# Kernel optimization log

Measured on AMD Instinct MI355X. Metric: run time of the kernel, lower is better.

The kernel has to match this reference:

```python
import jax, jax.numpy as jnp
from jax import lax
import numpy as np

B, C, H, W = 8, 256, 192, 192
ATT_K = 11
BN_EPS = 1e-5


def _dwconv(x, w, pad, stride=1):
    # x: NCHW, w: (C,1,kh,kw) depthwise
    return lax.conv_general_dilated(
        x, w, window_strides=(stride, stride), padding=pad,
        feature_group_count=x.shape[1],
        dimension_numbers=('NCHW', 'OIHW', 'NCHW'))


def _max_pool_3x3(x):
    return lax.reduce_window(x, -jnp.inf, lax.max,
                             (1, 1, 3, 3), (1, 1, 1, 1), 'SAME')


def _blur_pool(x, stride=3):
    # antialiased_cnns.BlurPool, filt_size=4: reflect pad [1,2,1,2], binomial 4x4, depthwise, stride 3
    c = x.shape[1]
    a = jnp.array([1., 3., 3., 1.], dtype=x.dtype)
    filt = (a[:, None] * a[None, :])
    filt = filt / jnp.sum(filt)
    w = jnp.tile(filt[None, None], (c, 1, 1, 1))  # (C,1,4,4)
    xp = jnp.pad(x, ((0, 0), (0, 0), (1, 2), (1, 2)), mode='reflect')
    return _dwconv(xp, w, 'VALID', stride=stride)


def _h_transform(x):
    b, c, h, w = x.shape
    x = jnp.pad(x, ((0, 0), (0, 0), (0, 0), (0, w)))
    x = x.reshape(b, c, -1)[..., :-w]
    return x.reshape(b, c, h, 2 * w - 1)


def _inv_h_transform(x):
    b, c, h, _ = x.shape  # last dim = 2h-1 (requires square)
    x = x.reshape(b, c, -1)
    x = jnp.pad(x, ((0, 0), (0, 0), (0, h)))
    x = x.reshape(b, c, h, 2 * h)
    return x[..., :h]


def _v_transform(x):
    return jnp.transpose(_h_transform(jnp.transpose(x, (0, 1, 3, 2))), (0, 1, 3, 2))


def _inv_v_transform(x):
    return jnp.transpose(_inv_h_transform(jnp.transpose(x, (0, 1, 3, 2))), (0, 1, 3, 2))


def setup_inputs() -> dict:
    key = jax.random.key(0)
    ks = jax.random.split(key, 5)
    pad = ATT_K // 2
    return {
        'x': jax.random.normal(ks[0], (B, C, H, W), dtype=jnp.float32),
        'w_h1': jax.random.normal(ks[1], (C, 1, ATT_K, 3), dtype=jnp.float32) * 0.1,
        'w_v1': jax.random.normal(ks[2], (C, 1, 3, ATT_K), dtype=jnp.float32) * 0.1,
        'w_h2': jax.random.normal(ks[3], (C, 1, ATT_K, 3), dtype=jnp.float32) * 0.1,
        'w_v2': jax.random.normal(ks[4], (C, 1, 3, ATT_K), dtype=jnp.float32) * 0.1,
        'bn_gamma': jnp.ones((C,), dtype=jnp.float32),
        'bn_beta': jnp.zeros((C,), dtype=jnp.float32),
        'bn_mean': jnp.zeros((C,), dtype=jnp.float32),
        'bn_var': jnp.ones((C,), dtype=jnp.float32),
    }


def reference(x, w_h1, w_v1, w_h2, w_v2, bn_gamma, bn_beta, bn_mean, bn_var):
    pad = ATT_K // 2
    b, c, h, w = x.shape

    x_tem = _max_pool_3x3(x)
    x_tem = _blur_pool(x_tem, stride=3)  # (B,C,64,64)

    x_h1 = _dwconv(x_tem, w_h1, ((pad, pad), (1, 1)))
    x_w1 = _dwconv(x_tem, w_v1, ((1, 1), (pad, pad)))

    # h == w (192 == 192): diagonal branch active
    x_h2 = _inv_h_transform(_dwconv(_h_transform(x_tem), w_h2, ((pad, pad), (1, 1))))
    x_w2 = _inv_v_transform(_dwconv(_v_transform(x_tem), w_v2, ((1, 1), (pad, pad))))

    s = x_h1 + x_w1 + x_h2 + x_w2
    # inference BatchNorm2d
    inv = bn_gamma / jnp.sqrt(bn_var + BN_EPS)
    att = (s - bn_mean[None, :, None, None]) * inv[None, :, None, None] + bn_beta[None, :, None, None]

    gate = jax.nn.sigmoid(att)
    # nearest interpolate to (h, w): idx = floor(i * in/out)
    ah, aw = gate.shape[2], gate.shape[3]
    idx_h = (jnp.arange(h) * ah) // h
    idx_w = (jnp.arange(w) * aw) // w
    gate_up = gate[:, :, idx_h][:, :, :, idx_w]

    return x[:, :c] * gate_up
```

## Files before the change

### kernel.cpp

```cpp
#include <hip/hip_runtime.h>
#include <hip/hip_fp16.h>
#include <math.h>

#define BN_EPS 1e-5f

__device__ __forceinline__ float max3f(float a, float b, float c) {
    return fmaxf(fmaxf(a, b), c);
}

__global__ __launch_bounds__(256, 8)
void mra_fused(const float* __restrict__ x,
               const float* __restrict__ wh1,
               const float* __restrict__ wv1,
               const float* __restrict__ wh2,
               const float* __restrict__ wv2,
               const float* __restrict__ bng,
               const float* __restrict__ bnb,
               const float* __restrict__ bnm,
               const float* __restrict__ bnv,
               float* __restrict__ out)
{
    __shared__ __align__(16) __half sxp_h[76][84];
    __shared__ __align__(16) float  rowbuf[4][2][192];

    const int plane = blockIdx.x;
    const int c     = plane & 255;
    const int tid   = threadIdx.x;
    const int lane  = tid & 63;
    const int wv    = tid >> 6;
    const float* __restrict__ xp = x   + (size_t)plane * 36864;
    float* __restrict__       op = out + (size_t)plane * 36864;

    {
        int* z = (int*)&sxp_h[0][0];
        #pragma unroll
        for (int i = 0; i < 13; ++i) {
            const int idx = tid + (i << 8);
            if (idx < (76 * 84 * 2) / 4) z[idx] = 0;
        }
    }
    __syncthreads();

    {
        const int P0 = wv << 4;
        float* rb0 = rowbuf[wv][0];
        float* rb1 = rowbuf[wv][1];
        const int i0 = (lane == 0) ? 1 : 3 * lane - 1;
        const int i1 = 3 * lane, i2 = 3 * lane + 1, i3 = 3 * lane + 2;
        const int r0 = 3 * P0 - 2;

        float4 ring[4];
        auto issue = [&](int k, float4* slot) {
            int r = r0 + k;
            r = r < 0 ? 0 : (r > 191 ? 191 : r);
            float4 v = make_float4(0.f, 0.f, 0.f, 0.f);
            if (lane < 48) v = *(const float4*)(xp + r * 192 + 4 * lane);
            *slot = v;
        };
        issue(0, &ring[0]); issue(1, &ring[1]);
        issue(2, &ring[2]); issue(3, &ring[3]);

        float h[3][4];
        float hb[3];
        float hbp = 0.f;

        #pragma unroll
        for (int k = 0; k < 51; ++k) {
            float4 v4 = ring[k & 3];
            if (k + 4 < 51) issue(k + 4, &ring[k & 3]);

            float nl = __shfl_up(v4.w, 1);
            float nr = __shfl_down(v4.x, 1);
            if (lane == 0)  nl = v4.x;
            if (lane == 47) nr = v4.w;
            float* rb = (k & 1) ? rb1 : rb0;
            if (lane < 48) {
                float4 hm;
                hm.x = max3f(nl,   v4.x, v4.y);
                hm.y = max3f(v4.x, v4.y, v4.z);
                hm.z = max3f(v4.y, v4.z, v4.w);
                hm.w = max3f(v4.z, v4.w, nr);
                *(float4*)(rb + 4 * lane) = hm;
            }
            __builtin_amdgcn_wave_barrier();
            float* hk = h[k % 3];
            hk[0] = rb[i0]; hk[1] = rb[i1]; hk[2] = rb[i2]; hk[3] = rb[i3];
            __builtin_amdgcn_wave_barrier();

            if (k >= 2) {
                const float* a = h[(k - 2) % 3];
                const float* b = h[(k - 1) % 3];
                const float* d = h[k % 3];
                const float e4 =
                      0.125f * max3f(a[0], b[0], d[0])
                    + 0.375f * max3f(a[1], b[1], d[1])
                    + 0.375f * max3f(a[2], b[2], d[2])
                    + 0.125f * max3f(a[3], b[3], d[3]);
                if (k == 2) {
                    hbp = e4;
                } else {
                    hb[k % 3] = e4;
                    if (k % 3 == 2) {
                        const int i = (k - 5) / 3;
                        float a_out;
                        if (i == 0 && wv == 0)
                            a_out = 0.375f * hb[0] + 0.5f * hb[1] + 0.125f * hb[2];
                        else
                            a_out = 0.125f * hbp + 0.375f * hb[0]
                                  + 0.375f * hb[1] + 0.125f * hb[2];
                        hbp = hb[2];
                        sxp_h[P0 + i + 6][lane + 8] = __float2half(a_out);
                    }
                }
            }
        }
    }
    __syncthreads();

    const int p  = tid >> 2;
    const int q0 = (tid & 3) << 4;
    float acc[16];
    #pragma unroll
    for (int i = 0; i < 16; ++i) acc[i] = 0.0f;

    const float* __restrict__ wh1p = wh1 + c * 33;
    const float* __restrict__ wv1p = wv1 + c * 33;
    const float* __restrict__ wh2p = wh2 + c * 33;
    const float* __restrict__ wv2p = wv2 + c * 33;

    #pragma unroll
    for (int e = -6; e <= 6; ++e) {
        float rbx[32];
        const __half* rowl = &sxp_h[p + e + 6][q0];
        #pragma unroll
        for (int u = 0; u < 8; ++u) {
            const __half2* h2p = (const __half2*)(rowl + 4 * u);
            const float2 f0 = __half22float2(h2p[0]);
            const float2 f1 = __half22float2(h2p[1]);
            rbx[4 * u + 0] = f0.x; rbx[4 * u + 1] = f0.y;
            rbx[4 * u + 2] = f1.x; rbx[4 * u + 3] = f1.y;
        }
        if (e >= -5 && e <= 5) {
            #pragma unroll
            for (int dw = -1; dw <= 1; ++dw) {
                const float wt = wh1p[(e + 5) * 3 + dw + 1];
                #pragma unroll
                for (int i = 0; i < 16; ++i) acc[i] += wt * rbx[i + dw + 8];
            }
            #pragma unroll
            for (int dw = -1; dw <= 1; ++dw) {
                const float wt = wh2p[(e + 5) * 3 + dw + 1];
                #pragma unroll
                for (int i = 0; i < 16; ++i) acc[i] += wt * rbx[i + dw - e + 8];
            }
        }
        if (e >= -1 && e <= 1) {
            #pragma unroll
            for (int dw = -5; dw <= 5; ++dw) {
                const float wt = wv1p[(e + 1) * 11 + dw + 5];
                #pragma unroll
                for (int i = 0; i < 16; ++i) acc[i] += wt * rbx[i + dw + 8];
            }
        }
        #pragma unroll
        for (int dh = -1; dh <= 1; ++dh) {
            const int dw = dh - e;
            if (dw >= -5 && dw <= 5) {
                const float wt = wv2p[(dh + 1) * 11 + dw + 5];
                #pragma unroll
                for (int i = 0; i < 16; ++i) acc[i] += wt * rbx[i + dh - e + 8];
            }
        }
    }

    const float inv = bng[c] * rsqrtf(bnv[c] + BN_EPS);
    const float mu  = bnm[c];
    const float bt  = bnb[c];
    __syncthreads();
    #pragma unroll
    for (int i = 0; i < 8; ++i) {
        const float a0 = (acc[2 * i]     - mu) * inv + bt;
        const float a1 = (acc[2 * i + 1] - mu) * inv + bt;
        const float g0 = 1.0f / (1.0f + __expf(-a0));
        const float g1 = 1.0f / (1.0f + __expf(-a1));
        *(__half2*)(&sxp_h[p + 6][q0 + 2 * i + 8]) = __floats2half2_rn(g0, g1);
    }
    __syncthreads();

    const float4* __restrict__ x4 = (const float4*)xp;
    float4* __restrict__       o4 = (float4*)op;
    int rowj[3], gcj[3], rrj[3];
    #pragma unroll
    for (int j = 0; j < 3; ++j) {
        const int idx0 = tid + (j << 8);
        const int rw   = idx0 / 48;
        const int c4   = idx0 - rw * 48;
        rowj[j] = rw;
        const int jb = c4 << 2;
        gcj[j] = jb / 3;
        rrj[j] = jb - 3 * gcj[j];
    }
    #pragma unroll
    for (int m = 0; m < 12; ++m) {
        #pragma unroll
        for (int j = 0; j < 3; ++j) {
            const int row = rowj[j] + (m << 4);
            const int idx = tid + ((m * 3 + j) << 8);
            const int gr  = row / 3 + 6;
            const float g0 = __half2float(sxp_h[gr][gcj[j] + 8]);
            const float g1 = __half2float(sxp_h[gr][gcj[j] + 9]);
            const float4 xv = x4[idx];
            float4 ov;
            const float s1 = (rrj[j] == 2) ? g1 : g0;
            const float s2 = (rrj[j] >= 1) ? g1 : g0;
            ov.x = xv.x * g0;
            ov.y = xv.y * s1;
            ov.z = xv.z * s2;
            ov.w = xv.w * g1;
            o4[idx] = ov;
        }
    }
}

extern "C" void kernel_launch(void* const* d_in, const int* in_sizes, int n_in,
                              void* d_out, int out_size, void* d_ws, size_t ws_size,
                              hipStream_t stream) {
    const float* x   = (const float*)d_in[0];
    const float* wh1 = (const float*)d_in[1];
    const float* wv1 = (const float*)d_in[2];
    const float* wh2 = (const float*)d_in[3];
    const float* wv2 = (const float*)d_in[4];
    const float* g   = (const float*)d_in[5];
    const float* b   = (const float*)d_in[6];
    const float* m   = (const float*)d_in[7];
    const float* v   = (const float*)d_in[8];

    mra_fused<<<dim3(8 * 256), dim3(256), 0, stream>>>(
        x, wh1, wv1, wh2, wv2, g, b, m, v, (float*)d_out);
}
```

Before: 175.1 us.

## Split each plane across two 128-thread blocks with recomputed halo rows

Each channel plane is now handled by two blocks of 128 threads, each covering half of the 64 pooled rows plus a 6-row halo. Each block recomputes the pooled halo rows itself. The goal is twice as many smaller blocks, for better occupancy and load balance with less shared memory per block. The cost is redundant max/blur pooling of the halo rows and extra global reads of x for the overlapping rows.

```diff
diff --git a/kernel.cpp b/kernel.cpp
--- a/kernel.cpp
+++ b/kernel.cpp
@@ -8,7 +8,7 @@
     return fmaxf(fmaxf(a, b), c);
 }
 
-__global__ __launch_bounds__(256, 8)
+__global__ __launch_bounds__(128, 8)
 void mra_fused(const float* __restrict__ x,
                const float* __restrict__ wh1,
                const float* __restrict__ wv1,
@@ -20,11 +20,14 @@
                const float* __restrict__ bnv,
                float* __restrict__ out)
 {
-    __shared__ __align__(16) __half sxp_h[76][84];
-    __shared__ __align__(16) float  rowbuf[4][2][192];
-
-    const int plane = blockIdx.x;
+    __shared__ __align__(16) __half sxp_h[44][84];
+    __shared__ __align__(16) float  rowbuf[2][2][192];
+
+    const int bid   = blockIdx.x;
+    const int plane = bid >> 1;
+    const int half  = bid & 1;
     const int c     = plane & 255;
+    const int B0    = half << 5;
     const int tid   = threadIdx.x;
     const int lane  = tid & 63;
     const int wv    = tid >> 6;
@@ -33,21 +36,22 @@
 
     {
         int* z = (int*)&sxp_h[0][0];
-        #pragma unroll
-        for (int i = 0; i < 13; ++i) {
-            const int idx = tid + (i << 8);
-            if (idx < (76 * 84 * 2) / 4) z[idx] = 0;
+        const int nInt = (44 * 84 * 2) / 4;
+        #pragma unroll
+        for (int i = 0; i < 15; ++i) {
+            const int idx = tid + (i << 7);
+            if (idx < nInt) z[idx] = 0;
         }
     }
     __syncthreads();
 
     {
-        const int P0 = wv << 4;
+        const int T0 = B0 - 6 + 22 * wv;
         float* rb0 = rowbuf[wv][0];
         float* rb1 = rowbuf[wv][1];
         const int i0 = (lane == 0) ? 1 : 3 * lane - 1;
         const int i1 = 3 * lane, i2 = 3 * lane + 1, i3 = 3 * lane + 2;
-        const int r0 = 3 * P0 - 2;
+        const int r0 = 3 * T0 - 2;
 
         float4 ring[4];
         auto issue = [&](int k, float4* slot) {
@@ -65,9 +69,9 @@
         float hbp = 0.f;
 
         #pragma unroll
-        for (int k = 0; k < 51; ++k) {
+        for (int k = 0; k < 69; ++k) {
             float4 v4 = ring[k & 3];
-            if (k + 4 < 51) issue(k + 4, &ring[k & 3]);
+            if (k + 4 < 69) issue(k + 4, &ring[k & 3]);
 
             float nl = __shfl_up(v4.w, 1);
             float nr = __shfl_down(v4.x, 1);
@@ -101,15 +105,16 @@
                 } else {
                     hb[k % 3] = e4;
                     if (k % 3 == 2) {
-                        const int i = (k - 5) / 3;
+                        const int t = T0 + (k - 5) / 3;
                         float a_out;
-                        if (i == 0 && wv == 0)
+                        if (t == 0)
                             a_out = 0.375f * hb[0] + 0.5f * hb[1] + 0.125f * hb[2];
                         else
                             a_out = 0.125f * hbp + 0.375f * hb[0]
                                   + 0.375f * hb[1] + 0.125f * hb[2];
                         hbp = hb[2];
-                        sxp_h[P0 + i + 6][lane + 8] = __float2half(a_out);
+                        if (t >= 0 && t <= 63)
+                            sxp_h[t - (B0 - 6)][lane + 8] = __float2half(a_out);
                     }
                 }
             }
@@ -117,8 +122,8 @@
     }
     __syncthreads();
 
-    const int p  = tid >> 2;
-    const int q0 = (tid & 3) << 4;
+    const int p_loc = tid >> 2;
+    const int q0    = (tid & 3) << 4;
     float acc[16];
     #pragma unroll
     for (int i = 0; i < 16; ++i) acc[i] = 0.0f;
@@ -131,7 +136,7 @@
     #pragma unroll
     for (int e = -6; e <= 6; ++e) {
         float rbx[32];
-        const __half* rowl = &sxp_h[p + e + 6][q0];
+        const __half* rowl = &sxp_h[p_loc + e + 6][q0];
         #pragma unroll
         for (int u = 0; u < 8; ++u) {
             const __half2* h2p = (const __half2*)(rowl + 4 * u);
@@ -183,16 +188,16 @@
         const float a1 = (acc[2 * i + 1] - mu) * inv + bt;
         const float g0 = 1.0f / (1.0f + __expf(-a0));
         const float g1 = 1.0f / (1.0f + __expf(-a1));
-        *(__half2*)(&sxp_h[p + 6][q0 + 2 * i + 8]) = __floats2half2_rn(g0, g1);
-    }
-    __syncthreads();
-
-    const float4* __restrict__ x4 = (const float4*)xp;
-    float4* __restrict__       o4 = (float4*)op;
+        *(__half2*)(&sxp_h[p_loc + 6][q0 + 2 * i + 8]) = __floats2half2_rn(g0, g1);
+    }
+    __syncthreads();
+
+    const float4* __restrict__ x4 = (const float4*)xp + half * (96 * 48);
+    float4* __restrict__       o4 = (float4*)op       + half * (96 * 48);
     int rowj[3], gcj[3], rrj[3];
     #pragma unroll
     for (int j = 0; j < 3; ++j) {
-        const int idx0 = tid + (j << 8);
+        const int idx0 = tid + (j << 7);
         const int rw   = idx0 / 48;
         const int c4   = idx0 - rw * 48;
         rowj[j] = rw;
@@ -204,8 +209,8 @@
     for (int m = 0; m < 12; ++m) {
         #pragma unroll
         for (int j = 0; j < 3; ++j) {
-            const int row = rowj[j] + (m << 4);
-            const int idx = tid + ((m * 3 + j) << 8);
+            const int row = rowj[j] + (m << 3);
+            const int idx = tid + ((m * 3 + j) << 7);
             const int gr  = row / 3 + 6;
             const float g0 = __half2float(sxp_h[gr][gcj[j] + 8]);
             const float g1 = __half2float(sxp_h[gr][gcj[j] + 9]);
@@ -235,6 +240,6 @@
     const float* m   = (const float*)d_in[7];
     const float* v   = (const float*)d_in[8];
 
-    mra_fused<<<dim3(8 * 256), dim3(256), 0, stream>>>(
+    mra_fused<<<dim3(2 * 8 * 256), dim3(128), 0, stream>>>(
         x, wh1, wv1, wh2, wv2, g, b, m, v, (float*)d_out);
 }
```

After: 202.0 us. 15.4% more time.
